# Kernel optimization log

Measured on AMD Instinct MI355X. Metric: run time of the kernel, lower is better.

Reference implementation:

```python
import jax, jax.numpy as jnp
import numpy as np

B, L, H = 16, 4096, 768

def setup_inputs() -> dict:
    key = jax.random.key(0)
    k1, k2 = jax.random.split(key)
    sequence_output = jax.random.normal(k1, (B, L, H), dtype=jnp.float32)
    # sorted segment ids: each wordpiece position maps to a token index in [0, L)
    wordpiece_to_token = jnp.sort(
        jax.random.randint(k2, (B, L), 0, L, dtype=jnp.int32), axis=-1)
    return {"sequence_output": sequence_output,
            "wordpiece_to_token": wordpiece_to_token}

def reference(sequence_output, wordpiece_to_token):
    # For each (batch, token j): output[b, j] = sum of sequence_output[b, p]
    # over wordpieces p assigned to token j. Tokens with no wordpieces stay 0,
    # matching torch.zeros_like initialization in the original.
    num_tokens = sequence_output.shape[1]
    def per_example(x, seg):  # x: [L, H], seg: [L]
        return jax.ops.segment_sum(x, seg, num_segments=num_tokens)
    return jax.vmap(per_example)(sequence_output, wordpiece_to_token)
```

## Files before the change

kernel.cpp:

```cpp
#include <hip/hip_runtime.h>

#define BB 16
#define LL 4096
#define H4 192

__global__ __launch_bounds__(256) void segsum_fused_kernel(
    const float4* __restrict__ x, const int* __restrict__ seg,
    float4* __restrict__ out) {
    int gtid = blockIdx.x * blockDim.x + threadIdx.x;
    int wave = gtid >> 6;
    int lane = gtid & 63;
    int b = wave >> 12;
    int j = wave & (LL - 1);

    const int* __restrict__ sb = seg + ((size_t)b << 12);

    int v1 = sb[lane << 6];
    unsigned long long ms = __ballot(v1 >= j);
    unsigned long long me = __ballot(v1 > j);

    int s, e;
    if (ms & 1ull) {
        s = 0;
    } else {
        int f = ms ? (__ffsll((unsigned long long)ms) - 1) : 64;
        int base = ((f - 1) << 6) + 1;
        int p2 = base + lane;
        int v2 = (p2 < LL) ? sb[p2] : 0x7fffffff;
        unsigned long long m2 = __ballot(v2 >= j);
        s = base + __ffsll(m2) - 1;
    }
    if (me & 1ull) {
        e = 0;
    } else {
        int f = me ? (__ffsll((unsigned long long)me) - 1) : 64;
        int base = ((f - 1) << 6) + 1;
        int p2 = base + lane;
        int v2 = (p2 < LL) ? sb[p2] : 0x7fffffff;
        unsigned long long m2 = __ballot(v2 > j);
        e = base + __ffsll(m2) - 1;
    }

    float4 a0 = make_float4(0.f, 0.f, 0.f, 0.f);
    float4 a1 = a0, a2 = a0;

    const float4* xb = x + (size_t)b * LL * H4;
    for (int p = s; p < e; ++p) {
        const float4* row = xb + (size_t)p * H4 + lane;
        float4 v0 = row[0];
        float4 vA = row[64];
        float4 vB = row[128];
        a0.x += v0.x; a0.y += v0.y; a0.z += v0.z; a0.w += v0.w;
        a1.x += vA.x; a1.y += vA.y; a1.z += vA.z; a1.w += vA.w;
        a2.x += vB.x; a2.y += vB.y; a2.z += vB.z; a2.w += vB.w;
    }

    float4* orow = out + (size_t)wave * H4 + lane;
    orow[0]   = a0;
    orow[64]  = a1;
    orow[128] = a2;
}

extern "C" void kernel_launch(void* const* d_in, const int* in_sizes, int n_in,
                              void* d_out, int out_size, void* d_ws, size_t ws_size,
                              hipStream_t stream) {
    const float* x   = (const float*)d_in[0];
    const int*   seg = (const int*)d_in[1];
    float* out = (float*)d_out;
    (void)d_ws; (void)ws_size;

    int nblocks = (BB * LL) / 4;
    segsum_fused_kernel<<<nblocks, 256, 0, stream>>>(
        (const float4*)x, seg, (float4*)out);
}
```

Before: 328.6 us.

## Precompute segment start offsets in a separate kernel and use nontemporal output stores

```diff
diff --git a/kernel.cpp b/kernel.cpp
--- a/kernel.cpp
+++ b/kernel.cpp
@@ -3,6 +3,59 @@
 #define BB 16
 #define LL 4096
 #define H4 192
+#define SP 4104
+
+typedef float nf4 __attribute__((ext_vector_type(4)));
+
+__global__ __launch_bounds__(256) void bounds_kernel(
+    const int* __restrict__ seg, int* __restrict__ starts) {
+    int b = blockIdx.x >> 4;
+    int p = ((blockIdx.x & 15) << 8) | threadIdx.x;
+    const int* __restrict__ sb = seg + (b << 12);
+    int* __restrict__ st = starts + b * SP;
+
+    int cur  = sb[p];
+    int prev = (p == 0) ? -1 : sb[p - 1];
+    for (int j = prev + 1; j <= cur; ++j) st[j] = p;
+    if (p == LL - 1)
+        for (int j = cur + 1; j <= LL; ++j) st[j] = LL;
+}
+
+__global__ __launch_bounds__(256) void segsum_bounds_kernel(
+    const float4* __restrict__ x, const int* __restrict__ starts,
+    float4* __restrict__ out) {
+    int gtid = blockIdx.x * blockDim.x + threadIdx.x;
+    int wave = gtid >> 6;
+    int lane = gtid & 63;
+    int b = wave >> 12;
+    int j = wave & (LL - 1);
+
+    const int* __restrict__ st = starts + b * SP + j;
+    int s = st[0];
+    int e = st[1];
+
+    float4 a0 = make_float4(0.f, 0.f, 0.f, 0.f);
+    float4 a1 = a0, a2 = a0;
+
+    const float4* xb = x + (size_t)b * LL * H4;
+    for (int p = s; p < e; ++p) {
+        const float4* row = xb + (size_t)p * H4 + lane;
+        float4 v0 = row[0];
+        float4 vA = row[64];
+        float4 vB = row[128];
+        a0.x += v0.x; a0.y += v0.y; a0.z += v0.z; a0.w += v0.w;
+        a1.x += vA.x; a1.y += vA.y; a1.z += vA.z; a1.w += vA.w;
+        a2.x += vB.x; a2.y += vB.y; a2.z += vB.z; a2.w += vB.w;
+    }
+
+    nf4* orow = (nf4*)(out + (size_t)wave * H4 + lane);
+    nf4 n0 = {a0.x, a0.y, a0.z, a0.w};
+    nf4 n1 = {a1.x, a1.y, a1.z, a1.w};
+    nf4 n2 = {a2.x, a2.y, a2.z, a2.w};
+    __builtin_nontemporal_store(n0, orow);
+    __builtin_nontemporal_store(n1, orow + 64);
+    __builtin_nontemporal_store(n2, orow + 128);
+}
 
 __global__ __launch_bounds__(256) void segsum_fused_kernel(
     const float4* __restrict__ x, const int* __restrict__ seg,
@@ -67,9 +120,15 @@
     const float* x   = (const float*)d_in[0];
     const int*   seg = (const int*)d_in[1];
     float* out = (float*)d_out;
-    (void)d_ws; (void)ws_size;
 
-    int nblocks = (BB * LL) / 4;
-    segsum_fused_kernel<<<nblocks, 256, 0, stream>>>(
-        (const float4*)x, seg, (float4*)out);
+    size_t need = (size_t)BB * SP * sizeof(int);
+    if (d_ws != nullptr && ws_size >= need) {
+        int* starts = (int*)d_ws;
+        bounds_kernel<<<BB * 16, 256, 0, stream>>>(seg, starts);
+        segsum_bounds_kernel<<<(BB * LL) / 4, 256, 0, stream>>>(
+            (const float4*)x, starts, (float4*)out);
+    } else {
+        segsum_fused_kernel<<<(BB * LL) / 4, 256, 0, stream>>>(
+            (const float4*)x, seg, (float4*)out);
+    }
 }
```

After: 343.2 us. 4.4% more time.

## Assign eight consecutive tokens per wave and share segment boundary searches

Applied to the files above, without the earlier changes.

```diff
diff --git a/kernel.cpp b/kernel.cpp
--- a/kernel.cpp
+++ b/kernel.cpp
@@ -3,62 +3,61 @@
 #define BB 16
 #define LL 4096
 #define H4 192
+#define TT 8
+#define LOG2T 3
 
-__global__ __launch_bounds__(256) void segsum_fused_kernel(
+__device__ __forceinline__ int lb64(const int* __restrict__ sb, int v1,
+                                    int j, int lane) {
+    unsigned long long m = __ballot(v1 >= j);
+    if (m & 1ull) return 0;
+    int f = m ? (__ffsll(m) - 1) : 64;
+    int base = ((f - 1) << 6) + 1;
+    int p2 = base + lane;
+    int v2 = (p2 < LL) ? sb[p2] : 0x7fffffff;
+    unsigned long long m2 = __ballot(v2 >= j);
+    return base + __ffsll(m2) - 1;
+}
+
+__global__ __launch_bounds__(256) void segsum_persist_kernel(
     const float4* __restrict__ x, const int* __restrict__ seg,
     float4* __restrict__ out) {
     int gtid = blockIdx.x * blockDim.x + threadIdx.x;
     int wave = gtid >> 6;
     int lane = gtid & 63;
-    int b = wave >> 12;
-    int j = wave & (LL - 1);
+    int b    = wave >> (12 - LOG2T);
+    int j0   = (wave & ((LL >> LOG2T) - 1)) << LOG2T;
 
     const int* __restrict__ sb = seg + ((size_t)b << 12);
 
     int v1 = sb[lane << 6];
-    unsigned long long ms = __ballot(v1 >= j);
-    unsigned long long me = __ballot(v1 > j);
+    int bound[TT + 1];
+    #pragma unroll
+    for (int i = 0; i <= TT; ++i)
+        bound[i] = lb64(sb, v1, j0 + i, lane);
 
-    int s, e;
-    if (ms & 1ull) {
-        s = 0;
-    } else {
-        int f = ms ? (__ffsll((unsigned long long)ms) - 1) : 64;
-        int base = ((f - 1) << 6) + 1;
-        int p2 = base + lane;
-        int v2 = (p2 < LL) ? sb[p2] : 0x7fffffff;
-        unsigned long long m2 = __ballot(v2 >= j);
-        s = base + __ffsll(m2) - 1;
+    const float4* __restrict__ xb = x + (size_t)b * (LL * H4);
+    float4* __restrict__ ob = out + ((size_t)(b << 12) + j0) * H4 + lane;
+
+    #pragma unroll
+    for (int i = 0; i < TT; ++i) {
+        int s = bound[i];
+        int e = bound[i + 1];
+        float4 a0 = make_float4(0.f, 0.f, 0.f, 0.f);
+        float4 a1 = a0, a2 = a0;
+        for (int p = s; p < e; ++p) {
+            const float4* row = xb + (size_t)p * H4 + lane;
+            float4 v0 = row[0];
+            float4 vA = row[64];
+            float4 vB = row[128];
+            a0.x += v0.x; a0.y += v0.y; a0.z += v0.z; a0.w += v0.w;
+            a1.x += vA.x; a1.y += vA.y; a1.z += vA.z; a1.w += vA.w;
+            a2.x += vB.x; a2.y += vB.y; a2.z += vB.z; a2.w += vB.w;
+        }
+        float4* orow = ob + (size_t)i * H4;
+        orow[0]   = a0;
+        orow[64]  = a1;
+        orow[128] = a2;
     }
-    if (me & 1ull) {
-        e = 0;
-    } else {
-        int f = me ? (__ffsll((unsigned long long)me) - 1) : 64;
-        int base = ((f - 1) << 6) + 1;
-        int p2 = base + lane;
-        int v2 = (p2 < LL) ? sb[p2] : 0x7fffffff;
-        unsigned long long m2 = __ballot(v2 > j);
-        e = base + __ffsll(m2) - 1;
-    }
-
-    float4 a0 = make_float4(0.f, 0.f, 0.f, 0.f);
-    float4 a1 = a0, a2 = a0;
-
-    const float4* xb = x + (size_t)b * LL * H4;
-    for (int p = s; p < e; ++p) {
-        const float4* row = xb + (size_t)p * H4 + lane;
-        float4 v0 = row[0];
-        float4 vA = row[64];
-        float4 vB = row[128];
-        a0.x += v0.x; a0.y += v0.y; a0.z += v0.z; a0.w += v0.w;
-        a1.x += vA.x; a1.y += vA.y; a1.z += vA.z; a1.w += vA.w;
-        a2.x += vB.x; a2.y += vB.y; a2.z += vB.z; a2.w += vB.w;
-    }
-
-    float4* orow = out + (size_t)wave * H4 + lane;
-    orow[0]   = a0;
-    orow[64]  = a1;
-    orow[128] = a2;
 }
 
 extern "C" void kernel_launch(void* const* d_in, const int* in_sizes, int n_in,
@@ -69,7 +68,7 @@
     float* out = (float*)d_out;
     (void)d_ws; (void)ws_size;
 
-    int nblocks = (BB * LL) / 4;
-    segsum_fused_kernel<<<nblocks, 256, 0, stream>>>(
+    int nblocks = (BB * (LL >> LOG2T)) / 4;
+    segsum_persist_kernel<<<nblocks, 256, 0, stream>>>(
         (const float4*)x, seg, (float4*)out);
 }
```

Result: slower. 344.5 us (+4.8%).
